# Kernel optimization log

Measured on AMD Instinct MI355X. Metric: run time of the kernel, lower is better.

Reference implementation:

```python
import jax, jax.numpy as jnp
import numpy as np

K = 32        # kernel_size = 64/(in_channels//32) with in_channels=64
STRIDE = 16   # kernel_size // 2
SIGMA = 32.0  # sigma = kernel_size
EPS = 1e-5
C = 64


def _gaussian(k, sigma, c):
    # torch.linspace(-k//2, k//2, k)
    v = jnp.linspace(-(k // 2), k // 2, k, dtype=jnp.float32)
    xx, yy = jnp.meshgrid(v, v, indexing='ij')
    g = jnp.exp(-(xx ** 2 + yy ** 2) / (2.0 * sigma ** 2)) + EPS  # (k,k)
    return jnp.broadcast_to(g[None], (c, k, k))  # (c,k,k)


def setup_inputs() -> dict:
    key = jax.random.key(0)
    x = jax.random.normal(key, (4, C, 384, 384), dtype=jnp.float32)
    return {"x": x}


def reference(x):
    b, c, h, w = x.shape
    nh = (h - K) // STRIDE + 1
    nw = (w - K) // STRIDE + 1
    g = _gaussian(K, SIGMA, c)  # (c,k,k)

    # window index map: R[i,p] = i*stride + p
    R = jnp.arange(nh)[:, None] * STRIDE + jnp.arange(K)[None, :]  # (nh,k)
    Cc = jnp.arange(nw)[:, None] * STRIDE + jnp.arange(K)[None, :]  # (nw,k)

    # unfold: gather overlapping patches -> (b,c,nh,k,nw,k)
    patches = x[:, :, R, :][:, :, :, :, Cc]

    # per-window, per-pixel normalization over the CHANNEL dim (unbiased std)
    mean = jnp.mean(patches, axis=1, keepdims=True)
    std = jnp.std(patches, axis=1, keepdims=True, ddof=1)
    normed = (patches - mean) / (std + EPS)

    # gaussian weighting per (c,k1,k2)
    weighted = normed * g[None, :, None, :, None, :]

    # fold: overlap-add scatter back to (b,c,h,w)
    out = jnp.zeros((b, c, h, w), dtype=x.dtype)
    out = out.at[:, :, R[:, :, None, None], Cc[None, None, :, :]].add(weighted)

    # counter = fold of gaussian weights (batch-independent)
    gpat = jnp.broadcast_to(g[:, None, :, None, :], (c, nh, K, nw, K))
    counter = jnp.zeros((c, h, w), dtype=x.dtype)
    counter = counter.at[:, R[:, :, None, None], Cc[None, None, :, :]].add(gpat)

    return out / counter[None]
```

## Files before the change

kernel.cpp:

```cpp
#include <hip/hip_runtime.h>


constexpr int B = 4;
constexpr int C = 64;
constexpr int H = 384;
constexpr int W = 384;
constexpr int HW = H * W;
constexpr int PIX_PER_BLK = 256;
constexpr float EPS = 1e-5f;

__global__ __launch_bounds__(256) void local_instance_norm_kernel(
    const float* __restrict__ x, float* __restrict__ out) {
    __shared__ float lds[C * PIX_PER_BLK];

    const int t = threadIdx.x;
    const int tile = blockIdx.x;
    const int b = tile / (HW / PIX_PER_BLK);
    const int s_base = (tile % (HW / PIX_PER_BLK)) * PIX_PER_BLK;

    const float* xp = x + (size_t)b * C * HW + s_base;
    float* op = out + (size_t)b * C * HW + s_base;

#pragma unroll
    for (int j = 0; j < 16; ++j) {
        int idx = j * 256 + t;
        int c = idx >> 6;
        int p4 = idx & 63;
        float4 val = *reinterpret_cast<const float4*>(xp + (size_t)c * HW + p4 * 4);
        *reinterpret_cast<float4*>(&lds[c * PIX_PER_BLK + p4 * 4]) = val;
    }
    __syncthreads();

    float sum = 0.f;
#pragma unroll
    for (int c = 0; c < C; ++c) sum += lds[c * PIX_PER_BLK + t];
    float mean = sum * (1.0f / C);

    float ss = 0.f;
#pragma unroll
    for (int c = 0; c < C; ++c) {
        float d = lds[c * PIX_PER_BLK + t] - mean;
        ss += d * d;
    }
    float var = ss * (1.0f / (C - 1));
    float inv = 1.0f / (sqrtf(var) + EPS);

#pragma unroll
    for (int c = 0; c < C; ++c) {
        op[(size_t)c * HW + t] = (lds[c * PIX_PER_BLK + t] - mean) * inv;
    }
}

extern "C" void kernel_launch(void* const* d_in, const int* in_sizes, int n_in,
                              void* d_out, int out_size, void* d_ws, size_t ws_size,
                              hipStream_t stream) {
    const float* x = (const float*)d_in[0];
    float* out = (float*)d_out;

    int grid = (B * HW) / PIX_PER_BLK;
    local_instance_norm_kernel<<<grid, 256, 0, stream>>>(x, out);
}
```

Baseline: 56.72 us.

## Keep channel tile in registers and use one-pass sum/sumsq stats

Drops the 64KB LDS staging buffer. Each thread now loads 16 float4 channel values straight into registers, and a small LDS array combines per-wave partial sums and sums of squares. The mean and unbiased variance are computed in a single pass from those sums, and the outputs are written as float4 stores. The aim is to remove LDS traffic and the occupancy limit caused by the large shared allocation on this memory-bound kernel. In exchange it uses more registers and carries the precision risk of the one-pass variance formula.

```diff
diff --git a/kernel.cpp b/kernel.cpp
--- a/kernel.cpp
+++ b/kernel.cpp
@@ -9,45 +9,72 @@
 constexpr int PIX_PER_BLK = 256;
 constexpr float EPS = 1e-5f;
 
-__global__ __launch_bounds__(256) void local_instance_norm_kernel(
+__global__ __launch_bounds__(256, 2) void local_instance_norm_kernel(
     const float* __restrict__ x, float* __restrict__ out) {
-    __shared__ float lds[C * PIX_PER_BLK];
+    __shared__ float4 ssum[4][64];
+    __shared__ float4 sssq[4][64];
 
     const int t = threadIdx.x;
+    const int w = t >> 6;
+    const int l = t & 63;
     const int tile = blockIdx.x;
     const int b = tile / (HW / PIX_PER_BLK);
     const int s_base = (tile % (HW / PIX_PER_BLK)) * PIX_PER_BLK;
 
-    const float* xp = x + (size_t)b * C * HW + s_base;
-    float* op = out + (size_t)b * C * HW + s_base;
+    const float* xp = x + (size_t)b * C * HW + s_base + 4 * l;
+    float* op = out + (size_t)b * C * HW + s_base + 4 * l;
+
+    float4 v[16];
+#pragma unroll
+    for (int j = 0; j < 16; ++j) {
+        v[j] = *reinterpret_cast<const float4*>(xp + (size_t)(4 * j + w) * HW);
+    }
+
+    float4 sum = make_float4(0.f, 0.f, 0.f, 0.f);
+    float4 ssq = make_float4(0.f, 0.f, 0.f, 0.f);
+#pragma unroll
+    for (int j = 0; j < 16; ++j) {
+        sum.x += v[j].x; sum.y += v[j].y; sum.z += v[j].z; sum.w += v[j].w;
+        ssq.x += v[j].x * v[j].x; ssq.y += v[j].y * v[j].y;
+        ssq.z += v[j].z * v[j].z; ssq.w += v[j].w * v[j].w;
+    }
+    ssum[w][l] = sum;
+    sssq[w][l] = ssq;
+    __syncthreads();
+
+    float4 S = make_float4(0.f, 0.f, 0.f, 0.f);
+    float4 Q = make_float4(0.f, 0.f, 0.f, 0.f);
+#pragma unroll
+    for (int ww = 0; ww < 4; ++ww) {
+        float4 a = ssum[ww][l];
+        float4 q = sssq[ww][l];
+        S.x += a.x; S.y += a.y; S.z += a.z; S.w += a.w;
+        Q.x += q.x; Q.y += q.y; Q.z += q.z; Q.w += q.w;
+    }
+
+    float4 mean, inv;
+    {
+        const float rn = 1.0f / C;
+        const float rn1 = 1.0f / (C - 1);
+        mean.x = S.x * rn; mean.y = S.y * rn; mean.z = S.z * rn; mean.w = S.w * rn;
+        float vx = fmaxf((Q.x - (float)C * mean.x * mean.x) * rn1, 0.f);
+        float vy = fmaxf((Q.y - (float)C * mean.y * mean.y) * rn1, 0.f);
+        float vz = fmaxf((Q.z - (float)C * mean.z * mean.z) * rn1, 0.f);
+        float vw = fmaxf((Q.w - (float)C * mean.w * mean.w) * rn1, 0.f);
+        inv.x = 1.0f / (sqrtf(vx) + EPS);
+        inv.y = 1.0f / (sqrtf(vy) + EPS);
+        inv.z = 1.0f / (sqrtf(vz) + EPS);
+        inv.w = 1.0f / (sqrtf(vw) + EPS);
+    }
 
 #pragma unroll
     for (int j = 0; j < 16; ++j) {
-        int idx = j * 256 + t;
-        int c = idx >> 6;
-        int p4 = idx & 63;
-        float4 val = *reinterpret_cast<const float4*>(xp + (size_t)c * HW + p4 * 4);
-        *reinterpret_cast<float4*>(&lds[c * PIX_PER_BLK + p4 * 4]) = val;
-    }
-    __syncthreads();
-
-    float sum = 0.f;
-#pragma unroll
-    for (int c = 0; c < C; ++c) sum += lds[c * PIX_PER_BLK + t];
-    float mean = sum * (1.0f / C);
-
-    float ss = 0.f;
-#pragma unroll
-    for (int c = 0; c < C; ++c) {
-        float d = lds[c * PIX_PER_BLK + t] - mean;
-        ss += d * d;
-    }
-    float var = ss * (1.0f / (C - 1));
-    float inv = 1.0f / (sqrtf(var) + EPS);
-
-#pragma unroll
-    for (int c = 0; c < C; ++c) {
-        op[(size_t)c * HW + t] = (lds[c * PIX_PER_BLK + t] - mean) * inv;
+        float4 o;
+        o.x = (v[j].x - mean.x) * inv.x;
+        o.y = (v[j].y - mean.y) * inv.y;
+        o.z = (v[j].z - mean.z) * inv.z;
+        o.w = (v[j].w - mean.w) * inv.w;
+        *reinterpret_cast<float4*>(op + (size_t)(4 * j + w) * HW) = o;
     }
 }
 
```

Measured after the change: 55.94 us. About the same (-1.4%).
